# Kernel optimization log

Hardware: AMD Instinct MI355X
Metric: run time of the kernel (lower is better)

Reference implementation:

```python
import jax, jax.numpy as jnp
import numpy as np
import math

HIDDEN = 1024
HEADS = 16
HEAD_DIM = HIDDEN // HEADS
B, S = 4, 2048


def setup_inputs() -> dict:
    key = jax.random.key(0)
    ks = jax.random.split(key, 9)
    std = 1.0 / math.sqrt(HIDDEN)
    return {
        "query": jax.random.normal(ks[0], (B, S, HIDDEN), jnp.float32),
        "key": jax.random.normal(ks[1], (B, S, HIDDEN), jnp.float32),
        "value": jax.random.normal(ks[2], (B, S, HIDDEN), jnp.float32),
        "q_w": jax.random.normal(ks[3], (HIDDEN, HIDDEN), jnp.float32) * std,
        "q_b": jax.random.normal(ks[4], (HIDDEN,), jnp.float32) * 0.02,
        "k_w": jax.random.normal(ks[5], (HIDDEN, HIDDEN), jnp.float32) * std,
        "k_b": jax.random.normal(ks[6], (HIDDEN,), jnp.float32) * 0.02,
        "v_w": jax.random.normal(ks[7], (HIDDEN, HIDDEN), jnp.float32) * std,
        "v_b": jax.random.normal(ks[8], (HIDDEN,), jnp.float32) * 0.02,
    }


def _split_heads(x):
    # [B, S, H] -> [B, heads, S, head_dim]
    b, s, _ = x.shape
    return x.reshape(b, s, HEADS, HEAD_DIM).transpose(0, 2, 1, 3)


def reference(query, key, value, q_w, q_b, k_w, k_b, v_w, v_b):
    # Linear projections (torch Linear: x @ W^T + b; here weights stored as [in, out])
    q = _split_heads(query @ q_w + q_b)   # [B, h, S, d]
    k = _split_heads(key @ k_w + k_b)
    v = _split_heads(value @ v_w + v_b)
    scale = 1.0 / math.sqrt(HEAD_DIM)
    scores = jnp.einsum("bhqd,bhkd->bhqk", q, k) * scale  # [B, h, S, S]
    # NOTE: faithful to source bug — context uses raw scaled scores, NOT softmax probs.
    # (softmax is computed in the original but its result is unused for the output.)
    ctx = jnp.einsum("bhqk,bhkd->bhqd", scores, v)
    ctx = ctx.transpose(0, 2, 1, 3).reshape(query.shape[0], query.shape[1], HIDDEN)
    return ctx
```

## Files before the change

kernel.cpp:

```cpp
#include <hip/hip_runtime.h>
#include <stdint.h>

#define HIDDEN 1024
#define HEADS 16
#define HEAD_DIM 64
#define BATCH 4
#define SEQ 2048
#define ROWS (BATCH * SEQ)

typedef float f32x4 __attribute__((ext_vector_type(4)));
typedef short bf16x8 __attribute__((ext_vector_type(8)));

__device__ __forceinline__ uint16_t f32_to_bf16_rne(float f) {
    uint32_t u = __float_as_uint(f);
    uint32_t r = u + 0x7FFFu + ((u >> 16) & 1u);
    return (uint16_t)(r >> 16);
}
__device__ __forceinline__ float bf16_to_f32(uint16_t u) {
    return __uint_as_float(((uint32_t)u) << 16);
}

__global__ __launch_bounds__(256) void cvt_kernel(const float* __restrict__ Xq,
                                                  const float* __restrict__ Xk,
                                                  const float* __restrict__ Xv,
                                                  uint16_t* __restrict__ Xb) {
    int z = blockIdx.x >> 13;
    const float* X = z == 0 ? Xq : (z == 1 ? Xk : Xv);
    uint16_t* out = Xb + (size_t)z * ROWS * HIDDEN;
    size_t i4 = (size_t)(blockIdx.x & 8191) * 256 + threadIdx.x;
    float4 f = ((const float4*)X)[i4];
    uint2 pk;
    pk.x = (uint32_t)f32_to_bf16_rne(f.x) | ((uint32_t)f32_to_bf16_rne(f.y) << 16);
    pk.y = (uint32_t)f32_to_bf16_rne(f.z) | ((uint32_t)f32_to_bf16_rne(f.w) << 16);
    ((uint2*)out)[i4] = pk;
}

__global__ __launch_bounds__(256) void wt_kernel(const float* __restrict__ Wk,
                                                 const float* __restrict__ Wv,
                                                 uint16_t* __restrict__ Wt) {
    const float* W = blockIdx.z == 0 ? Wk : Wv;
    uint16_t* out = Wt + (size_t)blockIdx.z * HIDDEN * HIDDEN;
    __shared__ float tile[64][65];
    int k0 = blockIdx.x * 64, n0 = blockIdx.y * 64;
    int r = threadIdx.x >> 6, c = threadIdx.x & 63;
    for (int it = 0; it < 16; ++it) {
        int rr = r + 4 * it;
        tile[rr][c] = W[(size_t)(k0 + rr) * HIDDEN + n0 + c];
    }
    __syncthreads();
    for (int it = 0; it < 16; ++it) {
        int rr = r + 4 * it;
        out[(size_t)(n0 + rr) * HIDDEN + k0 + c] = f32_to_bf16_rne(tile[c][rr]);
    }
}

__global__ __launch_bounds__(256) void proj_gemm(const uint16_t* __restrict__ Xkv,
                                                 const uint16_t* __restrict__ Wt,
                                                 const float* __restrict__ Bk,
                                                 const float* __restrict__ Bv,
                                                 uint16_t* __restrict__ KV) {
    const int z = blockIdx.z;
    const uint16_t* X = Xkv + (size_t)z * ROWS * HIDDEN;
    const uint16_t* W = Wt + (size_t)z * HIDDEN * HIDDEN;
    const float* bias = z == 0 ? Bk : Bv;
    uint16_t* out = KV + (size_t)z * ROWS * HIDDEN;

    __shared__ uint16_t slds[16384];

    const int tid = threadIdx.x;
    const int lane = tid & 63;
    const int w = tid >> 6;
    const int wm = (w >> 1) * 64;
    const int wn = (w & 1) * 64;
    const int m_lane = lane & 15;
    const int kq = lane >> 4;
    const int m0 = blockIdx.x * 128;
    const int n0 = blockIdx.y * 128;

    f32x4 acc[4][4] = {};

    for (int kb = 0; kb < HIDDEN; kb += 64) {
        for (int t = 0; t < 4; ++t) {
            int gbase = (w * 4 + t) * 64;
            int g = gbase + lane;
            int r = g >> 3;
            int c = (g & 7) ^ (r & 7);
            const uint16_t* srcA = X + (size_t)(m0 + r) * HIDDEN + kb + c * 8;
            __builtin_amdgcn_global_load_lds(
                (const __attribute__((address_space(1))) uint32_t*)srcA,
                (__attribute__((address_space(3))) uint32_t*)(&slds[gbase * 8]),
                16, 0, 0);
            const uint16_t* srcB = W + (size_t)(n0 + r) * HIDDEN + kb + c * 8;
            __builtin_amdgcn_global_load_lds(
                (const __attribute__((address_space(1))) uint32_t*)srcB,
                (__attribute__((address_space(3))) uint32_t*)(&slds[8192 + gbase * 8]),
                16, 0, 0);
        }
        __syncthreads();
        for (int ks = 0; ks < 2; ++ks) {
            int cbase = ks * 4 + kq;
            bf16x8 af[4], bfr[4];
            for (int i = 0; i < 4; ++i) {
                int r = wm + i * 16 + m_lane;
                int p = cbase ^ (r & 7);
                af[i] = *(const bf16x8*)(&slds[r * 64 + p * 8]);
            }
            for (int j = 0; j < 4; ++j) {
                int nr = wn + j * 16 + m_lane;
                int p = cbase ^ (nr & 7);
                bfr[j] = *(const bf16x8*)(&slds[8192 + nr * 64 + p * 8]);
            }
            for (int i = 0; i < 4; ++i)
                for (int j = 0; j < 4; ++j)
                    acc[i][j] = __builtin_amdgcn_mfma_f32_16x16x32_bf16(
                        af[i], bfr[j], acc[i][j], 0, 0, 0);
        }
        __syncthreads();
    }

    for (int j = 0; j < 4; ++j) {
        int col = n0 + wn + j * 16 + m_lane;
        float bj = bias[col];
        for (int i = 0; i < 4; ++i) {
            int rbase = m0 + wm + i * 16 + kq * 4;
            for (int rg = 0; rg < 4; ++rg) {
                float v = acc[i][j][rg] + bj;
                out[(size_t)(rbase + rg) * HIDDEN + col] = f32_to_bf16_rne(v);
            }
        }
    }
}

__global__ __launch_bounds__(256) void kv_kernel(const uint16_t* __restrict__ KV,
                                                 float* __restrict__ P) {
    const uint16_t* K = KV;
    const uint16_t* V = KV + (size_t)ROWS * HIDDEN;
    const int bh = blockIdx.x;
    const int sc = blockIdx.y;
    const int b = bh >> 4, h = bh & 15;
    const int tid = threadIdx.x;
    const size_t base = ((size_t)b * SEQ + sc * 256) * HIDDEN + h * 64;

    __shared__ float kk[16][64];
    __shared__ float vv[16][64];
    float acc[4][4] = {};
    const int i0 = (tid >> 4) * 4, j0 = (tid & 15) * 4;

    for (int batch = 0; batch < 16; ++batch) {
        __syncthreads();
        {
            int t = tid & 127;
            int row = t >> 3, c = t & 7;
            const uint16_t* src =
                (tid < 128 ? K : V) + base + (size_t)(batch * 16 + row) * HIDDEN + c * 8;
            float* dst = (tid < 128 ? &kk[row][c * 8] : &vv[row][c * 8]);
            bf16x8 d = *(const bf16x8*)src;
            for (int e = 0; e < 8; ++e) dst[e] = bf16_to_f32((uint16_t)d[e]);
        }
        __syncthreads();
        for (int r = 0; r < 16; ++r) {
            f32x4 ka = *(const f32x4*)(&kk[r][i0]);
            f32x4 va = *(const f32x4*)(&vv[r][j0]);
            for (int a = 0; a < 4; ++a)
                for (int bb = 0; bb < 4; ++bb)
                    acc[a][bb] += ka[a] * va[bb];
        }
    }
    float* Pp = P + ((size_t)bh * 8 + sc) * 4096;
    for (int a = 0; a < 4; ++a) {
        f32x4 row;
        for (int bb = 0; bb < 4; ++bb) row[bb] = acc[a][bb] * 0.125f;
        *(f32x4*)(&Pp[(i0 + a) * 64 + j0]) = row;
    }
}

__global__ __launch_bounds__(256) void wprime_kernel(const float* __restrict__ Wq,
                                                     const float* __restrict__ bq,
                                                     const float* __restrict__ P,
                                                     uint16_t* __restrict__ Wpt,
                                                     float* __restrict__ bp) {
    const int h = blockIdx.x;
    const int r0 = blockIdx.y * 64;
    const int b = blockIdx.z;
    const int tid = threadIdx.x;

    __shared__ float Mh[64][65];
    __shared__ float Wl[64][65];
    const float* Pp = P + ((size_t)(b * 16 + h)) * 8 * 4096;
    for (int it = 0; it < 16; ++it) {
        int e = it * 256 + tid;
        int a = e >> 6, c = e & 63;
        float s = 0.f;
        for (int sc = 0; sc < 8; ++sc) s += Pp[sc * 4096 + e];
        Mh[a][c] = s;
        Wl[a][c] = Wq[(size_t)(r0 + a) * HIDDEN + h * 64 + c];
    }
    __syncthreads();

    const int r = tid & 63;
    const int jbase = tid >> 6;
    float acc[16] = {};
    for (int i = 0; i < 64; ++i) {
        float wv = Wl[r][i];
        for (int jj = 0; jj < 16; ++jj)
            acc[jj] += wv * Mh[i][jbase + 4 * jj];
    }
    uint16_t* Wb = Wpt + (size_t)b * HIDDEN * HIDDEN;
    for (int jj = 0; jj < 16; ++jj) {
        int n = h * 64 + jbase + 4 * jj;
        Wb[(size_t)n * HIDDEN + r0 + r] = f32_to_bf16_rne(acc[jj]);
    }

    if (blockIdx.y == 0 && tid < 64) {
        int j = tid;
        float s = 0.f;
        for (int i = 0; i < 64; ++i) s += bq[h * 64 + i] * Mh[i][j];
        bp[b * HIDDEN + h * 64 + j] = s;
    }
}

__global__ __launch_bounds__(256) void final_gemm(const uint16_t* __restrict__ Xq,
                                                  const uint16_t* __restrict__ Wpt,
                                                  const float* __restrict__ bp,
                                                  float* __restrict__ out) {
    __shared__ uint16_t slds[16384];

    const int tid = threadIdx.x;
    const int lane = tid & 63;
    const int w = tid >> 6;
    const int wm = (w >> 1) * 64;
    const int wn = (w & 1) * 64;
    const int m_lane = lane & 15;
    const int kq = lane >> 4;
    const int m0 = blockIdx.x * 128;
    const int n0 = blockIdx.y * 128;
    const int batch = m0 >> 11;
    const uint16_t* W = Wpt + (size_t)batch * HIDDEN * HIDDEN;
    const float* bias = bp + batch * HIDDEN;

    f32x4 acc[4][4] = {};

    for (int kb = 0; kb < HIDDEN; kb += 64) {
        for (int t = 0; t < 4; ++t) {
            int gbase = (w * 4 + t) * 64;
            int g = gbase + lane;
            int r = g >> 3;
            int c = (g & 7) ^ (r & 7);
            const uint16_t* srcA = Xq + (size_t)(m0 + r) * HIDDEN + kb + c * 8;
            __builtin_amdgcn_global_load_lds(
                (const __attribute__((address_space(1))) uint32_t*)srcA,
                (__attribute__((address_space(3))) uint32_t*)(&slds[gbase * 8]),
                16, 0, 0);
            const uint16_t* srcB = W + (size_t)(n0 + r) * HIDDEN + kb + c * 8;
            __builtin_amdgcn_global_load_lds(
                (const __attribute__((address_space(1))) uint32_t*)srcB,
                (__attribute__((address_space(3))) uint32_t*)(&slds[8192 + gbase * 8]),
                16, 0, 0);
        }
        __syncthreads();
        for (int ks = 0; ks < 2; ++ks) {
            int cbase = ks * 4 + kq;
            bf16x8 af[4], bfr[4];
            for (int i = 0; i < 4; ++i) {
                int r = wm + i * 16 + m_lane;
                int p = cbase ^ (r & 7);
                af[i] = *(const bf16x8*)(&slds[r * 64 + p * 8]);
            }
            for (int j = 0; j < 4; ++j) {
                int nr = wn + j * 16 + m_lane;
                int p = cbase ^ (nr & 7);
                bfr[j] = *(const bf16x8*)(&slds[8192 + nr * 64 + p * 8]);
            }
            for (int i = 0; i < 4; ++i)
                for (int j = 0; j < 4; ++j)
                    acc[i][j] = __builtin_amdgcn_mfma_f32_16x16x32_bf16(
                        af[i], bfr[j], acc[i][j], 0, 0, 0);
        }
        __syncthreads();
    }

    for (int j = 0; j < 4; ++j) {
        int col = n0 + wn + j * 16 + m_lane;
        float bj = bias[col];
        for (int i = 0; i < 4; ++i) {
            int rbase = m0 + wm + i * 16 + kq * 4;
            for (int rg = 0; rg < 4; ++rg)
                out[(size_t)(rbase + rg) * HIDDEN + col] = acc[i][j][rg] + bj;
        }
    }
}

extern "C" void kernel_launch(void* const* d_in, const int* in_sizes, int n_in,
                              void* d_out, int out_size, void* d_ws, size_t ws_size,
                              hipStream_t stream) {
    const float* Xq = (const float*)d_in[0];
    const float* Xk = (const float*)d_in[1];
    const float* Xv = (const float*)d_in[2];
    const float* Wq = (const float*)d_in[3];
    const float* Bq = (const float*)d_in[4];
    const float* Wk = (const float*)d_in[5];
    const float* Bk = (const float*)d_in[6];
    const float* Wv = (const float*)d_in[7];
    const float* Bv = (const float*)d_in[8];
    float* out = (float*)d_out;

    char* ws = (char*)d_ws;
    uint16_t* Xb = (uint16_t*)ws;
    uint16_t* KV = (uint16_t*)(ws + 50331648);
    uint16_t* Wt = (uint16_t*)(ws + 83886080);
    float* P = (float*)(ws + 88080384);
    uint16_t* Wpt = (uint16_t*)(ws + 96468992);
    float* bp = (float*)(ws + 104857600);

    cvt_kernel<<<dim3(3 * 8192), 256, 0, stream>>>(Xq, Xk, Xv, Xb);
    wt_kernel<<<dim3(16, 16, 2), 256, 0, stream>>>(Wk, Wv, Wt);

    const uint16_t* Xkv = Xb + (size_t)ROWS * HIDDEN;
    proj_gemm<<<dim3(64, 8, 2), 256, 0, stream>>>(Xkv, Wt, Bk, Bv, KV);
    kv_kernel<<<dim3(64, 8), 256, 0, stream>>>(KV, P);
    wprime_kernel<<<dim3(16, 16, 4), 256, 0, stream>>>(Wq, Bq, P, Wpt, bp);
    final_gemm<<<dim3(64, 8), 256, 0, stream>>>(Xb, Wpt, bp, out);
}
```

Measured before the change: 269.7 us.

## Add pipelined 256x128 K-projection GEMM with direct-to-LDS loads

Adds a new K-projection GEMM kernel. It uses 512 threads and 256x128 tiles, double-buffers LDS filled by global_load_lds with an XOR swizzle, and interleaves MFMA with barriers and s_setprio. The V projection still runs on the old kernel as a separate launch. The aim is to raise MFMA utilisation and hide global-load latency in the projection GEMM. In exchange, the old single fused K+V launch becomes two serialized launches, and the new kernel runs at one block per CU with 96KB of dynamic LDS.

After: 272.1 us. No clear change (+0.9%).

```diff
diff --git a/kernel.cpp b/kernel.cpp
--- a/kernel.cpp
+++ b/kernel.cpp
@@ -51,6 +51,169 @@
     for (int it = 0; it < 16; ++it) {
         int rr = r + 4 * it;
         out[(size_t)(n0 + rr) * HIDDEN + k0 + c] = f32_to_bf16_rne(tile[c][rr]);
+    }
+}
+
+
+#define KSTAGE(GSRC, CHUNKBASE)                                                  \
+    {                                                                            \
+        _Pragma("unroll") for (int l = 0; l < 2; ++l) {                          \
+            int gb = l * 512 + w * 64;              \
+            int g = gb + lane;                                                   \
+            int r = g >> 3;                                                      \
+            int c = (g & 7) ^ (r & 7);                                           \
+            __builtin_amdgcn_global_load_lds(                                    \
+                (const __attribute__((address_space(1))) uint32_t*)((GSRC) +     \
+                    (size_t)r * HIDDEN + c * 8),                                 \
+                (__attribute__((address_space(3))) uint32_t*)(&lds[((CHUNKBASE) + gb) * 8]), \
+                16, 0, 0);                                                       \
+        }                                                                        \
+    }
+
+#define KLDA(BUF, MH)                                                            \
+    {                                                                            \
+        _Pragma("unroll") for (int fi = 0; fi < 2; ++fi) {                       \
+            int ar = wm + ((MH) * 2 + fi) * 16 + m_lane;                         \
+            _Pragma("unroll") for (int ks = 0; ks < 2; ++ks) {                   \
+                int p = (ks * 4 + kq) ^ (ar & 7);                                \
+                aq[fi][ks] = *(const bf16x8*)(&lds[(BUF) + ar * 64 + p * 8]);    \
+            }                                                                    \
+        }                                                                        \
+    }
+
+#define KLDB(BUF, NH, BQ)                                                        \
+    {                                                                            \
+        _Pragma("unroll") for (int fj = 0; fj < 2; ++fj) {                       \
+            int br = wn + ((NH) * 2 + fj) * 16 + m_lane;                         \
+            _Pragma("unroll") for (int ks = 0; ks < 2; ++ks) {                   \
+                int p = (ks * 4 + kq) ^ (br & 7);                                \
+                BQ[fj][ks] = *(const bf16x8*)(&lds[(BUF) + 16384 + br * 64 + p * 8]); \
+            }                                                                    \
+        }                                                                        \
+    }
+
+#define KMFMA(BQ, MH, NH)                                                        \
+    {                                                                            \
+        _Pragma("unroll") for (int ks = 0; ks < 2; ++ks)                         \
+        _Pragma("unroll") for (int fi = 0; fi < 2; ++fi)                         \
+        _Pragma("unroll") for (int fj = 0; fj < 2; ++fj)                         \
+            acc[(MH) * 2 + fi][(NH) * 2 + fj] =                                  \
+                __builtin_amdgcn_mfma_f32_16x16x32_bf16(                         \
+                    aq[fi][ks], BQ[fj][ks], acc[(MH) * 2 + fi][(NH) * 2 + fj], 0, 0, 0); \
+    }
+
+#define KMID()                                                                   \
+    __builtin_amdgcn_s_barrier();                                                \
+    asm volatile("s_waitcnt lgkmcnt(0)" ::: "memory");                           \
+    __builtin_amdgcn_s_setprio(1);
+
+#define KEND()                                                                   \
+    __builtin_amdgcn_s_setprio(0);                                               \
+    __builtin_amdgcn_s_barrier();
+
+#define B0A 0
+#define B0B 2048
+#define B1A 3072
+#define B1B 5120
+
+__global__ __launch_bounds__(512, 1) void projk8(const uint16_t* __restrict__ X,
+                                                 const uint16_t* __restrict__ W,
+                                                 const float* __restrict__ bias,
+                                                 uint16_t* __restrict__ out) {
+    extern __shared__ uint16_t lds[];
+
+    const int tid = threadIdx.x;
+    const int lane = tid & 63;
+    const int w = tid >> 6;
+    const int wm = (w >> 1) * 64;
+    const int wn = (w & 1) * 64;
+    const int m_lane = lane & 15;
+    const int kq = lane >> 4;
+    const int m0 = blockIdx.x * 256;
+    const int n0 = blockIdx.y * 128;
+
+    const uint16_t* Xb = X + (size_t)m0 * HIDDEN;
+    const uint16_t* Wb = W + (size_t)n0 * HIDDEN;
+
+    f32x4 acc[4][4] = {};
+    bf16x8 aq[2][2], b0q[2][2], b1q[2][2];
+
+    KSTAGE(Xb, B0A);
+    KSTAGE(Xb + 128 * HIDDEN, B0A + 1024);
+    KSTAGE(Wb, B0B);
+    KSTAGE(Wb + 64, B1B);
+    asm volatile("s_waitcnt vmcnt(2)" ::: "memory");
+    __builtin_amdgcn_s_barrier();
+
+#pragma unroll 1
+    for (int i = 0; i < 7; ++i) {
+        const int kb = i * 128;
+        KLDA(0, 0); KLDB(0, 0, b0q);
+        KSTAGE(Xb + kb + 64, B1A);
+        KMID(); KMFMA(b0q, 0, 0); KEND();
+        KLDB(0, 1, b1q);
+        KSTAGE(Xb + 128 * HIDDEN + kb + 64, B1A + 1024);
+        KMID(); KMFMA(b1q, 0, 1); KEND();
+        KLDA(0, 1);
+        KSTAGE(Wb + kb + 128, B0B);
+        KMID(); KMFMA(b1q, 1, 1); KEND();
+        asm volatile("s_waitcnt vmcnt(2)" ::: "memory");
+        __builtin_amdgcn_s_barrier();
+        __builtin_amdgcn_s_setprio(1);
+        KMFMA(b0q, 1, 0);
+        KEND();
+        KLDA(24576, 0); KLDB(24576, 0, b0q);
+        KSTAGE(Xb + kb + 128, B0A);
+        KMID(); KMFMA(b0q, 0, 0); KEND();
+        KLDB(24576, 1, b1q);
+        KSTAGE(Xb + 128 * HIDDEN + kb + 128, B0A + 1024);
+        KMID(); KMFMA(b1q, 0, 1); KEND();
+        KLDA(24576, 1);
+        KSTAGE(Wb + kb + 192, B1B);
+        KMID(); KMFMA(b1q, 1, 1); KEND();
+        asm volatile("s_waitcnt vmcnt(2)" ::: "memory");
+        __builtin_amdgcn_s_barrier();
+        __builtin_amdgcn_s_setprio(1);
+        KMFMA(b0q, 1, 0);
+        KEND();
+    }
+
+    {
+        const int kb = 896;
+        KLDA(0, 0); KLDB(0, 0, b0q);
+        KSTAGE(Xb + kb + 64, B1A);
+        KMID(); KMFMA(b0q, 0, 0); KEND();
+        KLDB(0, 1, b1q);
+        KSTAGE(Xb + 128 * HIDDEN + kb + 64, B1A + 1024);
+        KMID(); KMFMA(b1q, 0, 1); KEND();
+        KLDA(0, 1);
+        KMID(); KMFMA(b1q, 1, 1); KEND();
+        asm volatile("s_waitcnt vmcnt(0)" ::: "memory");
+        __builtin_amdgcn_s_barrier();
+        __builtin_amdgcn_s_setprio(1);
+        KMFMA(b0q, 1, 0);
+        KEND();
+        KLDA(24576, 0); KLDB(24576, 0, b0q);
+        KMID(); KMFMA(b0q, 0, 0); KEND();
+        KLDB(24576, 1, b1q);
+        KMID(); KMFMA(b1q, 0, 1); KEND();
+        KLDA(24576, 1);
+        KMID(); KMFMA(b1q, 1, 1); KEND();
+        __builtin_amdgcn_s_setprio(1);
+        KMFMA(b0q, 1, 0);
+        __builtin_amdgcn_s_setprio(0);
+    }
+
+    for (int fj = 0; fj < 4; ++fj) {
+        int col = n0 + wn + fj * 16 + m_lane;
+        float bj = bias[col];
+        for (int fi = 0; fi < 4; ++fi) {
+            int rbase = m0 + wm + fi * 16 + kq * 4;
+            for (int rg = 0; rg < 4; ++rg) {
+                float v = acc[fi][fj][rg] + bj;
+                out[(size_t)(rbase + rg) * HIDDEN + col] = f32_to_bf16_rne(v);
+            }
+        }
     }
 }
 
@@ -312,11 +475,22 @@
     uint16_t* Wpt = (uint16_t*)(ws + 96468992);
     float* bp = (float*)(ws + 104857600);
 
+    static bool attr_done = false;
+    if (!attr_done) {
+        (void)hipFuncSetAttribute((const void*)projk8,
+                                  hipFuncAttributeMaxDynamicSharedMemorySize, 98304);
+        attr_done = true;
+    }
+
     cvt_kernel<<<dim3(3 * 8192), 256, 0, stream>>>(Xq, Xk, Xv, Xb);
     wt_kernel<<<dim3(16, 16, 2), 256, 0, stream>>>(Wk, Wv, Wt);
 
     const uint16_t* Xkv = Xb + (size_t)ROWS * HIDDEN;
-    proj_gemm<<<dim3(64, 8, 2), 256, 0, stream>>>(Xkv, Wt, Bk, Bv, KV);
+    projk8<<<dim3(32, 8), 512, 98304, stream>>>(Xkv, Wt, Bk, KV);
+    proj_gemm<<<dim3(64, 8, 1), 256, 0, stream>>>(
+        Xkv + (size_t)ROWS * HIDDEN, Wt + (size_t)HIDDEN * HIDDEN, Bv, Bv,
+        KV + (size_t)ROWS * HIDDEN);
+
     kv_kernel<<<dim3(64, 8), 256, 0, stream>>>(KV, P);
     wprime_kernel<<<dim3(16, 16, 4), 256, 0, stream>>>(Wq, Bq, P, Wpt, bp);
     final_gemm<<<dim3(64, 8), 256, 0, stream>>>(Xb, Wpt, bp, out);
```

## Emit transposed K/V from projection and compute K^T V with MFMA

Applied to the files above, without the earlier changes.

The projection GEMM now swaps operands so it writes K and V transposed (hidden-major, sequence contiguous). The per-head K^T·V reduction then runs on bf16 MFMA instructions, with swizzled LDS tiles loaded via global_load_lds, in place of scalar FP32 outer products in shared memory. This removes an FP32 FMA bottleneck and the bf16-to-f32 conversion in kv_kernel. In exchange the projection epilogue stores are strided, since each lane writes a scattered bf16 element along columns.

After: 264.5 us. No clear change (-1.9%).

```diff
diff --git a/kernel.cpp b/kernel.cpp
--- a/kernel.cpp
+++ b/kernel.cpp
@@ -54,16 +54,16 @@
     }
 }
 
-__global__ __launch_bounds__(256) void proj_gemm(const uint16_t* __restrict__ Xkv,
-                                                 const uint16_t* __restrict__ Wt,
-                                                 const float* __restrict__ Bk,
-                                                 const float* __restrict__ Bv,
-                                                 uint16_t* __restrict__ KV) {
+__global__ __launch_bounds__(256) void proj_gemm_t(const uint16_t* __restrict__ Xkv,
+                                                   const uint16_t* __restrict__ Wt,
+                                                   const float* __restrict__ Bk,
+                                                   const float* __restrict__ Bv,
+                                                   uint16_t* __restrict__ KT) {
     const int z = blockIdx.z;
-    const uint16_t* X = Xkv + (size_t)z * ROWS * HIDDEN;
-    const uint16_t* W = Wt + (size_t)z * HIDDEN * HIDDEN;
+    const uint16_t* A = Wt + (size_t)z * HIDDEN * HIDDEN;
+    const uint16_t* B = Xkv + (size_t)z * ROWS * HIDDEN;
     const float* bias = z == 0 ? Bk : Bv;
-    uint16_t* out = KV + (size_t)z * ROWS * HIDDEN;
+    uint16_t* out = KT + (size_t)z * ROWS * HIDDEN;
 
     __shared__ uint16_t slds[16384];
 
@@ -85,12 +85,12 @@
             int g = gbase + lane;
             int r = g >> 3;
             int c = (g & 7) ^ (r & 7);
-            const uint16_t* srcA = X + (size_t)(m0 + r) * HIDDEN + kb + c * 8;
+            const uint16_t* srcA = A + (size_t)(m0 + r) * HIDDEN + kb + c * 8;
             __builtin_amdgcn_global_load_lds(
                 (const __attribute__((address_space(1))) uint32_t*)srcA,
                 (__attribute__((address_space(3))) uint32_t*)(&slds[gbase * 8]),
                 16, 0, 0);
-            const uint16_t* srcB = W + (size_t)(n0 + r) * HIDDEN + kb + c * 8;
+            const uint16_t* srcB = B + (size_t)(n0 + r) * HIDDEN + kb + c * 8;
             __builtin_amdgcn_global_load_lds(
                 (const __attribute__((address_space(1))) uint32_t*)srcB,
                 (__attribute__((address_space(3))) uint32_t*)(&slds[8192 + gbase * 8]),
@@ -118,59 +118,73 @@
         __syncthreads();
     }
 
-    for (int j = 0; j < 4; ++j) {
-        int col = n0 + wn + j * 16 + m_lane;
-        float bj = bias[col];
-        for (int i = 0; i < 4; ++i) {
-            int rbase = m0 + wm + i * 16 + kq * 4;
-            for (int rg = 0; rg < 4; ++rg) {
-                float v = acc[i][j][rg] + bj;
-                out[(size_t)(rbase + rg) * HIDDEN + col] = f32_to_bf16_rne(v);
-            }
-        }
-    }
-}
-
-__global__ __launch_bounds__(256) void kv_kernel(const uint16_t* __restrict__ KV,
-                                                 float* __restrict__ P) {
-    const uint16_t* K = KV;
-    const uint16_t* V = KV + (size_t)ROWS * HIDDEN;
+    for (int i = 0; i < 4; ++i) {
+        for (int rg = 0; rg < 4; ++rg) {
+            int row = m0 + wm + i * 16 + kq * 4 + rg;
+            float bj = bias[row];
+            for (int j = 0; j < 4; ++j) {
+                int col = n0 + wn + j * 16 + m_lane;
+                out[(size_t)row * ROWS + col] = f32_to_bf16_rne(acc[i][j][rg] + bj);
+            }
+        }
+    }
+}
+
+__global__ __launch_bounds__(256) void kv_mfma(const uint16_t* __restrict__ KT,
+                                               float* __restrict__ P) {
     const int bh = blockIdx.x;
     const int sc = blockIdx.y;
     const int b = bh >> 4, h = bh & 15;
+    const uint16_t* Kb = KT + (size_t)(h * 64) * ROWS + (size_t)b * SEQ + sc * 256;
+    const uint16_t* Vb = Kb + (size_t)HIDDEN * ROWS;
+
+    __shared__ uint16_t slds[8192];
+
     const int tid = threadIdx.x;
-    const size_t base = ((size_t)b * SEQ + sc * 256) * HIDDEN + h * 64;
-
-    __shared__ float kk[16][64];
-    __shared__ float vv[16][64];
-    float acc[4][4] = {};
-    const int i0 = (tid >> 4) * 4, j0 = (tid & 15) * 4;
-
-    for (int batch = 0; batch < 16; ++batch) {
-        __syncthreads();
-        {
-            int t = tid & 127;
-            int row = t >> 3, c = t & 7;
-            const uint16_t* src =
-                (tid < 128 ? K : V) + base + (size_t)(batch * 16 + row) * HIDDEN + c * 8;
-            float* dst = (tid < 128 ? &kk[row][c * 8] : &vv[row][c * 8]);
-            bf16x8 d = *(const bf16x8*)src;
-            for (int e = 0; e < 8; ++e) dst[e] = bf16_to_f32((uint16_t)d[e]);
-        }
-        __syncthreads();
-        for (int r = 0; r < 16; ++r) {
-            f32x4 ka = *(const f32x4*)(&kk[r][i0]);
-            f32x4 va = *(const f32x4*)(&vv[r][j0]);
-            for (int a = 0; a < 4; ++a)
-                for (int bb = 0; bb < 4; ++bb)
-                    acc[a][bb] += ka[a] * va[bb];
-        }
-    }
+    const int lane = tid & 63;
+    const int w = tid >> 6;
+    const int m_lane = lane & 15;
+    const int kq = lane >> 4;
+
+    f32x4 acc[4] = {};
+
+    for (int kb = 0; kb < 256; kb += 64) {
+        for (int t = 0; t < 2; ++t) {
+            int g = t * 256 + tid;
+            int r = g >> 3;
+            int c = (g & 7) ^ (r & 7);
+            const uint16_t* srcA = Kb + (size_t)r * ROWS + kb + c * 8;
+            __builtin_amdgcn_global_load_lds(
+                (const __attribute__((address_space(1))) uint32_t*)srcA,
+                (__attribute__((address_space(3))) uint32_t*)(&slds[g * 8]),
+                16, 0, 0);
+            const uint16_t* srcB = Vb + (size_t)r * ROWS + kb + c * 8;
+            __builtin_amdgcn_global_load_lds(
+                (const __attribute__((address_space(1))) uint32_t*)srcB,
+                (__attribute__((address_space(3))) uint32_t*)(&slds[4096 + g * 8]),
+                16, 0, 0);
+        }
+        __syncthreads();
+        for (int ks = 0; ks < 2; ++ks) {
+            int cbase = ks * 4 + kq;
+            int ar = w * 16 + m_lane;
+            bf16x8 af = *(const bf16x8*)(&slds[ar * 64 + (cbase ^ (ar & 7)) * 8]);
+            for (int j = 0; j < 4; ++j) {
+                int br = j * 16 + m_lane;
+                bf16x8 bf_ = *(const bf16x8*)(&slds[4096 + br * 64 + (cbase ^ (br & 7)) * 8]);
+                acc[j] = __builtin_amdgcn_mfma_f32_16x16x32_bf16(af, bf_, acc[j], 0, 0, 0);
+            }
+        }
+        __syncthreads();
+    }
+
     float* Pp = P + ((size_t)bh * 8 + sc) * 4096;
-    for (int a = 0; a < 4; ++a) {
-        f32x4 row;
-        for (int bb = 0; bb < 4; ++bb) row[bb] = acc[a][bb] * 0.125f;
-        *(f32x4*)(&Pp[(i0 + a) * 64 + j0]) = row;
+    for (int j = 0; j < 4; ++j) {
+        for (int rg = 0; rg < 4; ++rg) {
+            int row = w * 16 + kq * 4 + rg;
+            int col = j * 16 + m_lane;
+            Pp[row * 64 + col] = acc[j][rg] * 0.125f;
+        }
     }
 }
 
@@ -306,7 +320,7 @@
 
     char* ws = (char*)d_ws;
     uint16_t* Xb = (uint16_t*)ws;
-    uint16_t* KV = (uint16_t*)(ws + 50331648);
+    uint16_t* KT = (uint16_t*)(ws + 50331648);
     uint16_t* Wt = (uint16_t*)(ws + 83886080);
     float* P = (float*)(ws + 88080384);
     uint16_t* Wpt = (uint16_t*)(ws + 96468992);
@@ -316,8 +330,8 @@
     wt_kernel<<<dim3(16, 16, 2), 256, 0, stream>>>(Wk, Wv, Wt);
 
     const uint16_t* Xkv = Xb + (size_t)ROWS * HIDDEN;
-    proj_gemm<<<dim3(64, 8, 2), 256, 0, stream>>>(Xkv, Wt, Bk, Bv, KV);
-    kv_kernel<<<dim3(64, 8), 256, 0, stream>>>(KV, P);
+    proj_gemm_t<<<dim3(8, 64, 2), 256, 0, stream>>>(Xkv, Wt, Bk, Bv, KT);
+    kv_mfma<<<dim3(64, 8), 256, 0, stream>>>(KT, P);
     wprime_kernel<<<dim3(16, 16, 4), 256, 0, stream>>>(Wq, Bq, P, Wpt, bp);
     final_gemm<<<dim3(64, 8), 256, 0, stream>>>(Xb, Wpt, bp, out);
 }
```
